# Optimization experiments

Measured on AMD Instinct MI355X. Metric: run time of the kernel, lower is better.

The kernel has to match this reference:

```python
import jax, jax.numpy as jnp
import numpy as np

# BlendParams / camera defaults (pytorch3d)
SIGMA = 1e-4
GAMMA = 1e-4
ZNEAR = 1.0
ZFAR = 100.0
EPS_BLEND = 1e-10
BG = jnp.array([1.0, 1.0, 1.0], dtype=jnp.float32)

N, H, W, K = 8, 512, 512, 4
V, F = 50000, 100000


def _normalize(x, eps=1e-6):
    n = jnp.linalg.norm(x, axis=-1, keepdims=True)
    return x / jnp.maximum(n, eps)


def setup_inputs() -> dict:
    key = jax.random.key(0)
    ks = jax.random.split(key, 12)
    verts = jax.random.normal(ks[0], (V, 3), jnp.float32)
    vertex_normals = _normalize(jax.random.normal(ks[1], (V, 3), jnp.float32))
    faces = jax.random.randint(ks[2], (F, 3), 0, V)
    p2f = jax.random.randint(ks[3], (N, H, W, K), 0, F)
    drop = jax.random.uniform(ks[4], (N, H, W, K)) < 0.2
    pix_to_face = jnp.where(drop, -1, p2f)
    bary = jax.random.uniform(ks[5], (N, H, W, K, 3), jnp.float32, 1e-3, 1.0)
    bary_coords = bary / bary.sum(-1, keepdims=True)  # valid barycentric weights
    zbuf = jax.random.uniform(ks[6], (N, H, W, K), jnp.float32, ZNEAR, ZFAR)
    dists = jax.random.normal(ks[7], (N, H, W, K), jnp.float32) * 1e-3
    texels = jax.random.uniform(ks[8], (N, H, W, K, 3), jnp.float32)
    vis_maps = jax.random.uniform(ks[9], (N, H, W, 3), jnp.float32)
    light_location = jax.random.normal(ks[10], (N, 3), jnp.float32) * 3.0
    camera_center = jax.random.normal(ks[11], (N, 3), jnp.float32) * 5.0
    return dict(
        verts=verts, vertex_normals=vertex_normals, bary_coords=bary_coords,
        zbuf=zbuf, dists=dists, texels=texels, vis_maps=vis_maps,
        light_location=light_location,
        light_ambient=jnp.full((N, 3), 0.5, jnp.float32),
        light_diffuse=jnp.full((N, 3), 0.3, jnp.float32),
        light_specular=jnp.full((N, 3), 0.2, jnp.float32),
        camera_center=camera_center,
        mat_ambient=jnp.ones((N, 3), jnp.float32),
        mat_diffuse=jnp.ones((N, 3), jnp.float32),
        mat_specular=jnp.ones((N, 3), jnp.float32),
        shininess=jnp.full((N,), 64.0, jnp.float32),
        faces=faces, pix_to_face=pix_to_face,
    )


def _interpolate_face_attributes(pix_to_face, bary, face_attrs):
    # face_attrs: (F, 3, D); pix_to_face: (N,H,W,K); bary: (N,H,W,K,3)
    mask = pix_to_face < 0
    idx = jnp.where(mask, 0, pix_to_face)
    gathered = face_attrs[idx]  # (N,H,W,K,3,D)
    out = jnp.einsum('nhwkv,nhwkvd->nhwkd', bary, gathered)
    return jnp.where(mask[..., None], 0.0, out)


def reference(verts, vertex_normals, bary_coords, zbuf, dists, texels, vis_maps,
              light_location, light_ambient, light_diffuse, light_specular,
              camera_center, mat_ambient, mat_diffuse, mat_specular, shininess,
              faces, pix_to_face):
    faces_verts = verts[faces]            # (F,3,3)
    faces_normals = vertex_normals[faces]  # (F,3,3)
    pixel_coords = _interpolate_face_attributes(pix_to_face, bary_coords, faces_verts)
    pixel_normals = _interpolate_face_attributes(pix_to_face, bary_coords, faces_normals)

    # ---- Phong lighting (PointLights) ----
    b = lambda v: v[:, None, None, None, :]  # (N,3) -> (N,1,1,1,3)
    normals = _normalize(pixel_normals)
    direction = _normalize(b(light_location) - pixel_coords)
    cos_angle = jnp.sum(normals * direction, axis=-1)  # (N,H,W,K)
    diffuse_light = b(light_diffuse) * jax.nn.relu(cos_angle)[..., None]
    reflect = -direction + 2.0 * cos_angle[..., None] * normals
    view_dir = _normalize(b(camera_center) - pixel_coords)
    spec_cos = jax.nn.relu(jnp.sum(view_dir * reflect, axis=-1)) * (cos_angle > 0)
    spec_light = b(light_specular) * (spec_cos ** shininess[:, None, None, None])[..., None]
    ambient = b(mat_ambient * light_ambient)
    diffuse = b(mat_diffuse) * diffuse_light
    specular = b(mat_specular) * spec_light

    vis = vis_maps[:, :, :, None, :]  # broadcast over K (== unsqueeze(-2).repeat)
    colors = (ambient + diffuse * vis) * texels + specular  # (N,H,W,K,3)

    # ---- softmax_rgb_blend ----
    mask = (pix_to_face >= 0).astype(colors.dtype)
    prob_map = jax.nn.sigmoid(-dists / SIGMA) * mask
    alpha = 1.0 - jnp.prod(1.0 - prob_map, axis=-1)
    z_inv = (ZFAR - zbuf) / (ZFAR - ZNEAR) * mask
    z_inv_max = jnp.maximum(jnp.max(z_inv, axis=-1, keepdims=True), EPS_BLEND)
    weights_num = prob_map * jnp.exp((z_inv - z_inv_max) / GAMMA)
    delta = jnp.exp((EPS_BLEND - z_inv_max) / GAMMA)
    denom = jnp.sum(weights_num, axis=-1, keepdims=True) + delta
    weighted_colors = jnp.einsum('nhwk,nhwkc->nhwc', weights_num, colors)
    rgb = (weighted_colors + delta * BG) / denom
    return jnp.concatenate([rgb, alpha[..., None]], axis=-1)  # (N,H,W,4)
```

## Files before the change

### kernel.cpp

```cpp
#include <hip/hip_runtime.h>
#include <math.h>

#define SIGMA_C   1e-4f
#define GAMMA_C   1e-4f
#define ZNEAR_C   1.0f
#define ZFAR_C    100.0f
#define EPSB_C    1e-10f

static constexpr int N_ = 8, H_ = 512, W_ = 512, K_ = 4;
static constexpr int NPIX = N_ * H_ * W_;
static constexpr int HW_SHIFT = 18;
static constexpr int F_ = 100000;
static constexpr int REC_F = 20;
static constexpr size_t TABLE_BYTES = (size_t)F_ * REC_F * sizeof(float);

typedef float fvec4 __attribute__((ext_vector_type(4)));
typedef float fvec2 __attribute__((ext_vector_type(2)));
typedef int   ivec4 __attribute__((ext_vector_type(4)));

struct F3 { float x, y, z; };
struct I3 { int   x, y, z; };

__device__ __forceinline__ fvec4 ntload_f4(const float* p) {
    return __builtin_nontemporal_load(reinterpret_cast<const fvec4*>(p));
}
__device__ __forceinline__ ivec4 ntload_i4(const int* p) {
    return __builtin_nontemporal_load(reinterpret_cast<const ivec4*>(p));
}

__global__ __launch_bounds__(256) void build_face_table(
    const float* __restrict__ verts,
    const float* __restrict__ vnorm,
    const int*   __restrict__ faces,
    float* __restrict__ table)
{
    const int f = blockIdx.x * 256 + threadIdx.x;
    if (f >= F_) return;
    const int i0 = faces[3*f+0], i1 = faces[3*f+1], i2 = faces[3*f+2];
    const F3 a = reinterpret_cast<const F3*>(verts)[i0];
    const F3 b = reinterpret_cast<const F3*>(verts)[i1];
    const F3 c = reinterpret_cast<const F3*>(verts)[i2];
    const F3 p = reinterpret_cast<const F3*>(vnorm)[i0];
    const F3 q = reinterpret_cast<const F3*>(vnorm)[i1];
    const F3 r = reinterpret_cast<const F3*>(vnorm)[i2];
    float* o = table + (size_t)f * REC_F;
    fvec4 r0 = {a.x, a.y, a.z, b.x};
    fvec4 r1 = {b.y, b.z, c.x, c.y};
    fvec4 r2 = {c.z, p.x, p.y, p.z};
    fvec4 r3 = {q.x, q.y, q.z, r.x};
    fvec2 r4 = {r.y, r.z};
    *reinterpret_cast<fvec4*>(o + 0)  = r0;
    *reinterpret_cast<fvec4*>(o + 4)  = r1;
    *reinterpret_cast<fvec4*>(o + 8)  = r2;
    *reinterpret_cast<fvec4*>(o + 12) = r3;
    *reinterpret_cast<fvec2*>(o + 16) = r4;
}

__global__ __launch_bounds__(256) void soft_phong_kernel(
    const float* __restrict__ table,
    const float* __restrict__ bary,
    const float* __restrict__ zbuf,
    const float* __restrict__ dists,
    const float* __restrict__ texels,
    const float* __restrict__ vis,
    const float* __restrict__ l_loc,
    const float* __restrict__ l_amb,
    const float* __restrict__ l_dif,
    const float* __restrict__ l_spec,
    const float* __restrict__ cam,
    const float* __restrict__ m_amb,
    const float* __restrict__ m_dif,
    const float* __restrict__ m_spec,
    const float* __restrict__ shininess,
    const int*   __restrict__ p2f,
    float* __restrict__ out)
{
    const int p = blockIdx.x * 256 + threadIdx.x;
    const int n = p >> HW_SHIFT;

    const ivec4 f4 = ntload_i4(p2f + 4*p);
    const fvec4 z4 = ntload_f4(zbuf + 4*p);
    const fvec4 d4 = ntload_f4(dists + 4*p);
    const fvec4 bA = ntload_f4(bary + 12*p + 0);
    const fvec4 bB = ntload_f4(bary + 12*p + 4);
    const fvec4 bC = ntload_f4(bary + 12*p + 8);
    const fvec4 tA = ntload_f4(texels + 12*p + 0);
    const fvec4 tB = ntload_f4(texels + 12*p + 4);
    const fvec4 tC = ntload_f4(texels + 12*p + 8);
    const float vR = __builtin_nontemporal_load(vis + 3*p+0);
    const float vG = __builtin_nontemporal_load(vis + 3*p+1);
    const float vB = __builtin_nontemporal_load(vis + 3*p+2);

    const int fi[4] = {f4.x, f4.y, f4.z, f4.w};

    const float llx = l_loc[3*n+0], lly = l_loc[3*n+1], llz = l_loc[3*n+2];
    const float ccx = cam[3*n+0],   ccy = cam[3*n+1],   ccz = cam[3*n+2];
    const float ambR = m_amb[3*n+0]*l_amb[3*n+0];
    const float ambG = m_amb[3*n+1]*l_amb[3*n+1];
    const float ambB = m_amb[3*n+2]*l_amb[3*n+2];
    const float kdR  = m_dif[3*n+0]*l_dif[3*n+0];
    const float kdG  = m_dif[3*n+1]*l_dif[3*n+1];
    const float kdB  = m_dif[3*n+2]*l_dif[3*n+2];
    const float ksR  = m_spec[3*n+0]*l_spec[3*n+0];
    const float ksG  = m_spec[3*n+1]*l_spec[3*n+1];
    const float ksB  = m_spec[3*n+2]*l_spec[3*n+2];
    const float shin = shininess[n];

    const float zb[4] = {z4.x, z4.y, z4.z, z4.w};
    const float dd[4] = {d4.x, d4.y, d4.z, d4.w};
    const float bc[12] = {bA.x,bA.y,bA.z,bA.w, bB.x,bB.y,bB.z,bB.w, bC.x,bC.y,bC.z,bC.w};
    const float tx[12] = {tA.x,tA.y,tA.z,tA.w, tB.x,tB.y,tB.z,tB.w, tC.x,tC.y,tC.z,tC.w};

    float colR[4], colG[4], colB[4], prob[4], zinv[4];
    float zmax = EPSB_C;

#pragma unroll
    for (int k = 0; k < 4; ++k) {
        const bool live = fi[k] >= 0;
        const int  f    = live ? fi[k] : 0;
        const float* rec = table + (size_t)f * REC_F;
        const fvec4 r0 = *reinterpret_cast<const fvec4*>(rec + 0);
        const fvec4 r1 = *reinterpret_cast<const fvec4*>(rec + 4);
        const fvec4 r2 = *reinterpret_cast<const fvec4*>(rec + 8);
        const fvec4 r3 = *reinterpret_cast<const fvec4*>(rec + 12);
        const fvec2 r4 = *reinterpret_cast<const fvec2*>(rec + 16);

        const float b0 = bc[3*k+0], b1 = bc[3*k+1], b2 = bc[3*k+2];

        const float pcx = b0*r0.x + b1*r0.w + b2*r1.z;
        const float pcy = b0*r0.y + b1*r1.x + b2*r1.w;
        const float pcz = b0*r0.z + b1*r1.y + b2*r2.x;

        const float pnx = b0*r2.y + b1*r3.x + b2*r3.w;
        const float pny = b0*r2.z + b1*r3.y + b2*r4.x;
        const float pnz = b0*r2.w + b1*r3.z + b2*r4.y;

        const float nl  = sqrtf(pnx*pnx + pny*pny + pnz*pnz);
        const float inl = 1.0f / fmaxf(nl, 1e-6f);
        const float nx = pnx*inl, ny = pny*inl, nz = pnz*inl;

        float dx = llx - pcx, dy = lly - pcy, dz = llz - pcz;
        const float dl  = sqrtf(dx*dx + dy*dy + dz*dz);
        const float idl = 1.0f / fmaxf(dl, 1e-6f);
        dx *= idl; dy *= idl; dz *= idl;

        const float cosang = nx*dx + ny*dy + nz*dz;
        const float rcos   = fmaxf(cosang, 0.0f);

        const float rx = 2.0f*cosang*nx - dx;
        const float ry = 2.0f*cosang*ny - dy;
        const float rz = 2.0f*cosang*nz - dz;

        float vx = ccx - pcx, vy = ccy - pcy, vz = ccz - pcz;
        const float vl  = sqrtf(vx*vx + vy*vy + vz*vz);
        const float ivl = 1.0f / fmaxf(vl, 1e-6f);
        vx *= ivl; vy *= ivl; vz *= ivl;

        const float sdot = vx*rx + vy*ry + vz*rz;
        const float spec_cos = (cosang > 0.0f) ? fmaxf(sdot, 0.0f) : 0.0f;
        const float sp = (spec_cos > 0.0f) ? exp2f(shin * log2f(spec_cos)) : 0.0f;

        colR[k] = (ambR + kdR*rcos*vR) * tx[3*k+0] + ksR*sp;
        colG[k] = (ambG + kdG*rcos*vG) * tx[3*k+1] + ksG*sp;
        colB[k] = (ambB + kdB*rcos*vB) * tx[3*k+2] + ksB*sp;

        prob[k] = live ? 1.0f / (1.0f + __expf(dd[k] / SIGMA_C)) : 0.0f;
        zinv[k] = live ? (ZFAR_C - zb[k]) / (ZFAR_C - ZNEAR_C)  : 0.0f;
        zmax = fmaxf(zmax, zinv[k]);
    }

    const float delta = __expf((EPSB_C - zmax) / GAMMA_C);
    float denom = delta;
    float accR = delta, accG = delta, accB = delta;
    float keep = 1.0f;
#pragma unroll
    for (int k = 0; k < 4; ++k) {
        const float w = prob[k] * __expf((zinv[k] - zmax) / GAMMA_C);
        denom += w;
        accR += w * colR[k];
        accG += w * colG[k];
        accB += w * colB[k];
        keep *= (1.0f - prob[k]);
    }
    const float inv = 1.0f / denom;
    fvec4 res; res.x = accR*inv; res.y = accG*inv; res.z = accB*inv; res.w = 1.0f - keep;
    __builtin_nontemporal_store(res, reinterpret_cast<fvec4*>(out) + p);
}

__global__ __launch_bounds__(256) void soft_phong_direct(
    const float* __restrict__ verts,
    const float* __restrict__ vnorm,
    const float* __restrict__ bary,
    const float* __restrict__ zbuf,
    const float* __restrict__ dists,
    const float* __restrict__ texels,
    const float* __restrict__ vis,
    const float* __restrict__ l_loc,
    const float* __restrict__ l_amb,
    const float* __restrict__ l_dif,
    const float* __restrict__ l_spec,
    const float* __restrict__ cam,
    const float* __restrict__ m_amb,
    const float* __restrict__ m_dif,
    const float* __restrict__ m_spec,
    const float* __restrict__ shininess,
    const int*   __restrict__ faces,
    const int*   __restrict__ p2f,
    float* __restrict__ out)
{
    const int p = blockIdx.x * 256 + threadIdx.x;
    const int n = p >> HW_SHIFT;
    const ivec4 f4 = ntload_i4(p2f + 4*p);
    const fvec4 z4 = ntload_f4(zbuf + 4*p);
    const fvec4 d4 = ntload_f4(dists + 4*p);
    const fvec4 bA = ntload_f4(bary + 12*p + 0);
    const fvec4 bB = ntload_f4(bary + 12*p + 4);
    const fvec4 bC = ntload_f4(bary + 12*p + 8);
    const fvec4 tA = ntload_f4(texels + 12*p + 0);
    const fvec4 tB = ntload_f4(texels + 12*p + 4);
    const fvec4 tC = ntload_f4(texels + 12*p + 8);
    const float vR = vis[3*p+0], vG = vis[3*p+1], vB = vis[3*p+2];
    const int fi[4] = {f4.x, f4.y, f4.z, f4.w};
    I3 fidx[4];
#pragma unroll
    for (int k = 0; k < 4; ++k) {
        const int f = (fi[k] >= 0) ? fi[k] : 0;
        fidx[k] = reinterpret_cast<const I3*>(faces)[f];
    }
    F3 vp[4][3], vn[4][3];
#pragma unroll
    for (int k = 0; k < 4; ++k) {
        const int i0 = fidx[k].x, i1 = fidx[k].y, i2 = fidx[k].z;
        vp[k][0] = reinterpret_cast<const F3*>(verts)[i0];
        vp[k][1] = reinterpret_cast<const F3*>(verts)[i1];
        vp[k][2] = reinterpret_cast<const F3*>(verts)[i2];
        vn[k][0] = reinterpret_cast<const F3*>(vnorm)[i0];
        vn[k][1] = reinterpret_cast<const F3*>(vnorm)[i1];
        vn[k][2] = reinterpret_cast<const F3*>(vnorm)[i2];
    }
    const float llx = l_loc[3*n+0], lly = l_loc[3*n+1], llz = l_loc[3*n+2];
    const float ccx = cam[3*n+0],   ccy = cam[3*n+1],   ccz = cam[3*n+2];
    const float ambR = m_amb[3*n+0]*l_amb[3*n+0];
    const float ambG = m_amb[3*n+1]*l_amb[3*n+1];
    const float ambB = m_amb[3*n+2]*l_amb[3*n+2];
    const float kdR  = m_dif[3*n+0]*l_dif[3*n+0];
    const float kdG  = m_dif[3*n+1]*l_dif[3*n+1];
    const float kdB  = m_dif[3*n+2]*l_dif[3*n+2];
    const float ksR  = m_spec[3*n+0]*l_spec[3*n+0];
    const float ksG  = m_spec[3*n+1]*l_spec[3*n+1];
    const float ksB  = m_spec[3*n+2]*l_spec[3*n+2];
    const float shin = shininess[n];
    const float zb[4] = {z4.x, z4.y, z4.z, z4.w};
    const float dd[4] = {d4.x, d4.y, d4.z, d4.w};
    const float bc[12] = {bA.x,bA.y,bA.z,bA.w, bB.x,bB.y,bB.z,bB.w, bC.x,bC.y,bC.z,bC.w};
    const float tx[12] = {tA.x,tA.y,tA.z,tA.w, tB.x,tB.y,tB.z,tB.w, tC.x,tC.y,tC.z,tC.w};
    float colR[4], colG[4], colB[4], prob[4], zinv[4];
    float zmax = EPSB_C;
#pragma unroll
    for (int k = 0; k < 4; ++k) {
        const bool live = fi[k] >= 0;
        const float b0 = bc[3*k+0], b1 = bc[3*k+1], b2 = bc[3*k+2];
        const float pcx = b0*vp[k][0].x + b1*vp[k][1].x + b2*vp[k][2].x;
        const float pcy = b0*vp[k][0].y + b1*vp[k][1].y + b2*vp[k][2].y;
        const float pcz = b0*vp[k][0].z + b1*vp[k][1].z + b2*vp[k][2].z;
        const float pnx = b0*vn[k][0].x + b1*vn[k][1].x + b2*vn[k][2].x;
        const float pny = b0*vn[k][0].y + b1*vn[k][1].y + b2*vn[k][2].y;
        const float pnz = b0*vn[k][0].z + b1*vn[k][1].z + b2*vn[k][2].z;
        const float nl  = sqrtf(pnx*pnx + pny*pny + pnz*pnz);
        const float inl = 1.0f / fmaxf(nl, 1e-6f);
        const float nx = pnx*inl, ny = pny*inl, nz = pnz*inl;
        float dx = llx - pcx, dy = lly - pcy, dz = llz - pcz;
        const float dl  = sqrtf(dx*dx + dy*dy + dz*dz);
        const float idl = 1.0f / fmaxf(dl, 1e-6f);
        dx *= idl; dy *= idl; dz *= idl;
        const float cosang = nx*dx + ny*dy + nz*dz;
        const float rcos   = fmaxf(cosang, 0.0f);
        const float rx = 2.0f*cosang*nx - dx;
        const float ry = 2.0f*cosang*ny - dy;
        const float rz = 2.0f*cosang*nz - dz;
        float vx = ccx - pcx, vy = ccy - pcy, vz = ccz - pcz;
        const float vl  = sqrtf(vx*vx + vy*vy + vz*vz);
        const float ivl = 1.0f / fmaxf(vl, 1e-6f);
        vx *= ivl; vy *= ivl; vz *= ivl;
        const float sdot = vx*rx + vy*ry + vz*rz;
        const float spec_cos = (cosang > 0.0f) ? fmaxf(sdot, 0.0f) : 0.0f;
        const float sp = (spec_cos > 0.0f) ? exp2f(shin * log2f(spec_cos)) : 0.0f;
        colR[k] = (ambR + kdR*rcos*vR) * tx[3*k+0] + ksR*sp;
        colG[k] = (ambG + kdG*rcos*vG) * tx[3*k+1] + ksG*sp;
        colB[k] = (ambB + kdB*rcos*vB) * tx[3*k+2] + ksB*sp;
        prob[k] = live ? 1.0f / (1.0f + __expf(dd[k] / SIGMA_C)) : 0.0f;
        zinv[k] = live ? (ZFAR_C - zb[k]) / (ZFAR_C - ZNEAR_C)  : 0.0f;
        zmax = fmaxf(zmax, zinv[k]);
    }
    const float delta = __expf((EPSB_C - zmax) / GAMMA_C);
    float denom = delta;
    float accR = delta, accG = delta, accB = delta;
    float keep = 1.0f;
#pragma unroll
    for (int k = 0; k < 4; ++k) {
        const float w = prob[k] * __expf((zinv[k] - zmax) / GAMMA_C);
        denom += w;
        accR += w * colR[k];
        accG += w * colG[k];
        accB += w * colB[k];
        keep *= (1.0f - prob[k]);
    }
    const float inv = 1.0f / denom;
    fvec4 res; res.x = accR*inv; res.y = accG*inv; res.z = accB*inv; res.w = 1.0f - keep;
    __builtin_nontemporal_store(res, reinterpret_cast<fvec4*>(out) + p);
}

extern "C" void kernel_launch(void* const* d_in, const int* in_sizes, int n_in,
                              void* d_out, int out_size, void* d_ws, size_t ws_size,
                              hipStream_t stream) {
    const float* verts   = (const float*)d_in[0];
    const float* vnorm   = (const float*)d_in[1];
    const float* bary    = (const float*)d_in[2];
    const float* zbuf    = (const float*)d_in[3];
    const float* dists   = (const float*)d_in[4];
    const float* texels  = (const float*)d_in[5];
    const float* vis     = (const float*)d_in[6];
    const float* l_loc   = (const float*)d_in[7];
    const float* l_amb   = (const float*)d_in[8];
    const float* l_dif   = (const float*)d_in[9];
    const float* l_spec  = (const float*)d_in[10];
    const float* cam     = (const float*)d_in[11];
    const float* m_amb   = (const float*)d_in[12];
    const float* m_dif   = (const float*)d_in[13];
    const float* m_spec  = (const float*)d_in[14];
    const float* shin    = (const float*)d_in[15];
    const int*   faces   = (const int*)d_in[16];
    const int*   p2f     = (const int*)d_in[17];
    float* out = (float*)d_out;

    if (ws_size >= TABLE_BYTES) {
        float* table = (float*)d_ws;
        build_face_table<<<(F_ + 255) / 256, 256, 0, stream>>>(verts, vnorm, faces, table);
        soft_phong_kernel<<<NPIX / 256, 256, 0, stream>>>(
            table, bary, zbuf, dists, texels, vis,
            l_loc, l_amb, l_dif, l_spec, cam,
            m_amb, m_dif, m_spec, shin, p2f, out);
    } else {
        soft_phong_direct<<<NPIX / 256, 256, 0, stream>>>(
            verts, vnorm, bary, zbuf, dists, texels, vis,
            l_loc, l_amb, l_dif, l_spec, cam,
            m_amb, m_dif, m_spec, shin, faces, p2f, out);
    }
}
```

Measured before the change: 410.6 us.

## Map one thread per fragment sample and blend across lanes with shuffles

The main kernel now assigns one thread to each (pixel, k) fragment rather than one thread per pixel looping over four fragments. The softmax blend reduction (max, sums, product) is done with xor-shuffles across groups of four lanes, and each lane writes one output channel. The aim is more parallelism and more outstanding independent face-table gathers to hide the latency of random accesses. In exchange it uses scalar rather than vector loads for per-sample inputs, loads vis redundantly per lane, and adds shuffle overhead. The fallback direct kernel is also reworked to use scalar loads.

```diff
diff --git a/kernel.cpp b/kernel.cpp
--- a/kernel.cpp
+++ b/kernel.cpp
@@ -9,23 +9,18 @@
 
 static constexpr int N_ = 8, H_ = 512, W_ = 512, K_ = 4;
 static constexpr int NPIX = N_ * H_ * W_;
-static constexpr int HW_SHIFT = 18;
+static constexpr int NSMP = NPIX * K_;
 static constexpr int F_ = 100000;
 static constexpr int REC_F = 20;
 static constexpr size_t TABLE_BYTES = (size_t)F_ * REC_F * sizeof(float);
 
 typedef float fvec4 __attribute__((ext_vector_type(4)));
 typedef float fvec2 __attribute__((ext_vector_type(2)));
-typedef int   ivec4 __attribute__((ext_vector_type(4)));
 
 struct F3 { float x, y, z; };
-struct I3 { int   x, y, z; };
-
-__device__ __forceinline__ fvec4 ntload_f4(const float* p) {
-    return __builtin_nontemporal_load(reinterpret_cast<const fvec4*>(p));
-}
-__device__ __forceinline__ ivec4 ntload_i4(const int* p) {
-    return __builtin_nontemporal_load(reinterpret_cast<const ivec4*>(p));
+
+__device__ __forceinline__ float ntf(const float* p) {
+    return __builtin_nontemporal_load(p);
 }
 
 __global__ __launch_bounds__(256) void build_face_table(
@@ -56,7 +51,7 @@
     *reinterpret_cast<fvec2*>(o + 16) = r4;
 }
 
-__global__ __launch_bounds__(256) void soft_phong_kernel(
+__global__ __launch_bounds__(256) void soft_phong_sample(
     const float* __restrict__ table,
     const float* __restrict__ bary,
     const float* __restrict__ zbuf,
@@ -75,23 +70,26 @@
     const int*   __restrict__ p2f,
     float* __restrict__ out)
 {
-    const int p = blockIdx.x * 256 + threadIdx.x;
-    const int n = p >> HW_SHIFT;
-
-    const ivec4 f4 = ntload_i4(p2f + 4*p);
-    const fvec4 z4 = ntload_f4(zbuf + 4*p);
-    const fvec4 d4 = ntload_f4(dists + 4*p);
-    const fvec4 bA = ntload_f4(bary + 12*p + 0);
-    const fvec4 bB = ntload_f4(bary + 12*p + 4);
-    const fvec4 bC = ntload_f4(bary + 12*p + 8);
-    const fvec4 tA = ntload_f4(texels + 12*p + 0);
-    const fvec4 tB = ntload_f4(texels + 12*p + 4);
-    const fvec4 tC = ntload_f4(texels + 12*p + 8);
-    const float vR = __builtin_nontemporal_load(vis + 3*p+0);
-    const float vG = __builtin_nontemporal_load(vis + 3*p+1);
-    const float vB = __builtin_nontemporal_load(vis + 3*p+2);
-
-    const int fi[4] = {f4.x, f4.y, f4.z, f4.w};
+    const int s = blockIdx.x * 256 + threadIdx.x;
+    const int p = s >> 2;
+    const int k = s & 3;
+    const int n = s >> 20;
+
+    const int  f0   = __builtin_nontemporal_load(p2f + s);
+    const bool live = f0 >= 0;
+    const int  f    = live ? f0 : 0;
+    const float* rec = table + (size_t)f * REC_F;
+    const fvec4 r0 = *reinterpret_cast<const fvec4*>(rec + 0);
+    const fvec4 r1 = *reinterpret_cast<const fvec4*>(rec + 4);
+    const fvec4 r2 = *reinterpret_cast<const fvec4*>(rec + 8);
+    const fvec4 r3 = *reinterpret_cast<const fvec4*>(rec + 12);
+    const fvec2 r4 = *reinterpret_cast<const fvec2*>(rec + 16);
+
+    const float zb = ntf(zbuf + s);
+    const float dd = ntf(dists + s);
+    const float b0 = ntf(bary + 3*s+0), b1 = ntf(bary + 3*s+1), b2 = ntf(bary + 3*s+2);
+    const float t0 = ntf(texels + 3*s+0), t1 = ntf(texels + 3*s+1), t2 = ntf(texels + 3*s+2);
+    const float vR = vis[3*p+0], vG = vis[3*p+1], vB = vis[3*p+2];
 
     const float llx = l_loc[3*n+0], lly = l_loc[3*n+1], llz = l_loc[3*n+2];
     const float ccx = cam[3*n+0],   ccy = cam[3*n+1],   ccz = cam[3*n+2];
@@ -106,85 +104,70 @@
     const float ksB  = m_spec[3*n+2]*l_spec[3*n+2];
     const float shin = shininess[n];
 
-    const float zb[4] = {z4.x, z4.y, z4.z, z4.w};
-    const float dd[4] = {d4.x, d4.y, d4.z, d4.w};
-    const float bc[12] = {bA.x,bA.y,bA.z,bA.w, bB.x,bB.y,bB.z,bB.w, bC.x,bC.y,bC.z,bC.w};
-    const float tx[12] = {tA.x,tA.y,tA.z,tA.w, tB.x,tB.y,tB.z,tB.w, tC.x,tC.y,tC.z,tC.w};
-
-    float colR[4], colG[4], colB[4], prob[4], zinv[4];
-    float zmax = EPSB_C;
-
-#pragma unroll
-    for (int k = 0; k < 4; ++k) {
-        const bool live = fi[k] >= 0;
-        const int  f    = live ? fi[k] : 0;
-        const float* rec = table + (size_t)f * REC_F;
-        const fvec4 r0 = *reinterpret_cast<const fvec4*>(rec + 0);
-        const fvec4 r1 = *reinterpret_cast<const fvec4*>(rec + 4);
-        const fvec4 r2 = *reinterpret_cast<const fvec4*>(rec + 8);
-        const fvec4 r3 = *reinterpret_cast<const fvec4*>(rec + 12);
-        const fvec2 r4 = *reinterpret_cast<const fvec2*>(rec + 16);
-
-        const float b0 = bc[3*k+0], b1 = bc[3*k+1], b2 = bc[3*k+2];
-
-        const float pcx = b0*r0.x + b1*r0.w + b2*r1.z;
-        const float pcy = b0*r0.y + b1*r1.x + b2*r1.w;
-        const float pcz = b0*r0.z + b1*r1.y + b2*r2.x;
-
-        const float pnx = b0*r2.y + b1*r3.x + b2*r3.w;
-        const float pny = b0*r2.z + b1*r3.y + b2*r4.x;
-        const float pnz = b0*r2.w + b1*r3.z + b2*r4.y;
-
-        const float nl  = sqrtf(pnx*pnx + pny*pny + pnz*pnz);
-        const float inl = 1.0f / fmaxf(nl, 1e-6f);
-        const float nx = pnx*inl, ny = pny*inl, nz = pnz*inl;
-
-        float dx = llx - pcx, dy = lly - pcy, dz = llz - pcz;
-        const float dl  = sqrtf(dx*dx + dy*dy + dz*dz);
-        const float idl = 1.0f / fmaxf(dl, 1e-6f);
-        dx *= idl; dy *= idl; dz *= idl;
-
-        const float cosang = nx*dx + ny*dy + nz*dz;
-        const float rcos   = fmaxf(cosang, 0.0f);
-
-        const float rx = 2.0f*cosang*nx - dx;
-        const float ry = 2.0f*cosang*ny - dy;
-        const float rz = 2.0f*cosang*nz - dz;
-
-        float vx = ccx - pcx, vy = ccy - pcy, vz = ccz - pcz;
-        const float vl  = sqrtf(vx*vx + vy*vy + vz*vz);
-        const float ivl = 1.0f / fmaxf(vl, 1e-6f);
-        vx *= ivl; vy *= ivl; vz *= ivl;
-
-        const float sdot = vx*rx + vy*ry + vz*rz;
-        const float spec_cos = (cosang > 0.0f) ? fmaxf(sdot, 0.0f) : 0.0f;
-        const float sp = (spec_cos > 0.0f) ? exp2f(shin * log2f(spec_cos)) : 0.0f;
-
-        colR[k] = (ambR + kdR*rcos*vR) * tx[3*k+0] + ksR*sp;
-        colG[k] = (ambG + kdG*rcos*vG) * tx[3*k+1] + ksG*sp;
-        colB[k] = (ambB + kdB*rcos*vB) * tx[3*k+2] + ksB*sp;
-
-        prob[k] = live ? 1.0f / (1.0f + __expf(dd[k] / SIGMA_C)) : 0.0f;
-        zinv[k] = live ? (ZFAR_C - zb[k]) / (ZFAR_C - ZNEAR_C)  : 0.0f;
-        zmax = fmaxf(zmax, zinv[k]);
-    }
+    const float pcx = b0*r0.x + b1*r0.w + b2*r1.z;
+    const float pcy = b0*r0.y + b1*r1.x + b2*r1.w;
+    const float pcz = b0*r0.z + b1*r1.y + b2*r2.x;
+
+    const float pnx = b0*r2.y + b1*r3.x + b2*r3.w;
+    const float pny = b0*r2.z + b1*r3.y + b2*r4.x;
+    const float pnz = b0*r2.w + b1*r3.z + b2*r4.y;
+
+    const float nl  = sqrtf(pnx*pnx + pny*pny + pnz*pnz);
+    const float inl = 1.0f / fmaxf(nl, 1e-6f);
+    const float nx = pnx*inl, ny = pny*inl, nz = pnz*inl;
+
+    float dx = llx - pcx, dy = lly - pcy, dz = llz - pcz;
+    const float dl  = sqrtf(dx*dx + dy*dy + dz*dz);
+    const float idl = 1.0f / fmaxf(dl, 1e-6f);
+    dx *= idl; dy *= idl; dz *= idl;
+
+    const float cosang = nx*dx + ny*dy + nz*dz;
+    const float rcos   = fmaxf(cosang, 0.0f);
+
+    const float rx = 2.0f*cosang*nx - dx;
+    const float ry = 2.0f*cosang*ny - dy;
+    const float rz = 2.0f*cosang*nz - dz;
+
+    float vx = ccx - pcx, vy = ccy - pcy, vz = ccz - pcz;
+    const float vl  = sqrtf(vx*vx + vy*vy + vz*vz);
+    const float ivl = 1.0f / fmaxf(vl, 1e-6f);
+    vx *= ivl; vy *= ivl; vz *= ivl;
+
+    const float sdot = vx*rx + vy*ry + vz*rz;
+    const float spec_cos = (cosang > 0.0f) ? fmaxf(sdot, 0.0f) : 0.0f;
+    const float sp = (spec_cos > 0.0f) ? exp2f(shin * log2f(spec_cos)) : 0.0f;
+
+    const float colR = (ambR + kdR*rcos*vR) * t0 + ksR*sp;
+    const float colG = (ambG + kdG*rcos*vG) * t1 + ksG*sp;
+    const float colB = (ambB + kdB*rcos*vB) * t2 + ksB*sp;
+
+    const float prob = live ? 1.0f / (1.0f + __expf(dd / SIGMA_C)) : 0.0f;
+    const float zinv = live ? (ZFAR_C - zb) / (ZFAR_C - ZNEAR_C)  : 0.0f;
+
+    float zmax = zinv;
+    zmax = fmaxf(zmax, __shfl_xor(zmax, 1));
+    zmax = fmaxf(zmax, __shfl_xor(zmax, 2));
+    zmax = fmaxf(zmax, EPSB_C);
+
+    const float w = prob * __expf((zinv - zmax) / GAMMA_C);
+    float aw = w, aR = w*colR, aG = w*colG, aB = w*colB, kp = 1.0f - prob;
+
+    aw += __shfl_xor(aw, 1);  aR += __shfl_xor(aR, 1);
+    aG += __shfl_xor(aG, 1);  aB += __shfl_xor(aB, 1);
+    kp *= __shfl_xor(kp, 1);
+    aw += __shfl_xor(aw, 2);  aR += __shfl_xor(aR, 2);
+    aG += __shfl_xor(aG, 2);  aB += __shfl_xor(aB, 2);
+    kp *= __shfl_xor(kp, 2);
 
     const float delta = __expf((EPSB_C - zmax) / GAMMA_C);
-    float denom = delta;
-    float accR = delta, accG = delta, accB = delta;
-    float keep = 1.0f;
-#pragma unroll
-    for (int k = 0; k < 4; ++k) {
-        const float w = prob[k] * __expf((zinv[k] - zmax) / GAMMA_C);
-        denom += w;
-        accR += w * colR[k];
-        accG += w * colG[k];
-        accB += w * colB[k];
-        keep *= (1.0f - prob[k]);
-    }
-    const float inv = 1.0f / denom;
-    fvec4 res; res.x = accR*inv; res.y = accG*inv; res.z = accB*inv; res.w = 1.0f - keep;
-    __builtin_nontemporal_store(res, reinterpret_cast<fvec4*>(out) + p);
+    const float inv   = 1.0f / (aw + delta);
+
+    float val;
+    if      (k == 0) val = (aR + delta) * inv;
+    else if (k == 1) val = (aG + delta) * inv;
+    else if (k == 2) val = (aB + delta) * inv;
+    else             val = 1.0f - kp;
+    __builtin_nontemporal_store(val, out + s);
 }
 
 __global__ __launch_bounds__(256) void soft_phong_direct(
@@ -209,18 +192,9 @@
     float* __restrict__ out)
 {
     const int p = blockIdx.x * 256 + threadIdx.x;
-    const int n = p >> HW_SHIFT;
-    const ivec4 f4 = ntload_i4(p2f + 4*p);
-    const fvec4 z4 = ntload_f4(zbuf + 4*p);
-    const fvec4 d4 = ntload_f4(dists + 4*p);
-    const fvec4 bA = ntload_f4(bary + 12*p + 0);
-    const fvec4 bB = ntload_f4(bary + 12*p + 4);
-    const fvec4 bC = ntload_f4(bary + 12*p + 8);
-    const fvec4 tA = ntload_f4(texels + 12*p + 0);
-    const fvec4 tB = ntload_f4(texels + 12*p + 4);
-    const fvec4 tC = ntload_f4(texels + 12*p + 8);
-    const float vR = vis[3*p+0], vG = vis[3*p+1], vB = vis[3*p+2];
-    const int fi[4] = {f4.x, f4.y, f4.z, f4.w};
+    const int n = p >> 18;
+    struct I3 { int x, y, z; };
+    const int fi[4] = {p2f[4*p+0], p2f[4*p+1], p2f[4*p+2], p2f[4*p+3]};
     I3 fidx[4];
 #pragma unroll
     for (int k = 0; k < 4; ++k) {
@@ -250,16 +224,12 @@
     const float ksG  = m_spec[3*n+1]*l_spec[3*n+1];
     const float ksB  = m_spec[3*n+2]*l_spec[3*n+2];
     const float shin = shininess[n];
-    const float zb[4] = {z4.x, z4.y, z4.z, z4.w};
-    const float dd[4] = {d4.x, d4.y, d4.z, d4.w};
-    const float bc[12] = {bA.x,bA.y,bA.z,bA.w, bB.x,bB.y,bB.z,bB.w, bC.x,bC.y,bC.z,bC.w};
-    const float tx[12] = {tA.x,tA.y,tA.z,tA.w, tB.x,tB.y,tB.z,tB.w, tC.x,tC.y,tC.z,tC.w};
     float colR[4], colG[4], colB[4], prob[4], zinv[4];
     float zmax = EPSB_C;
 #pragma unroll
     for (int k = 0; k < 4; ++k) {
         const bool live = fi[k] >= 0;
-        const float b0 = bc[3*k+0], b1 = bc[3*k+1], b2 = bc[3*k+2];
+        const float b0 = bary[12*p+3*k+0], b1 = bary[12*p+3*k+1], b2 = bary[12*p+3*k+2];
         const float pcx = b0*vp[k][0].x + b1*vp[k][1].x + b2*vp[k][2].x;
         const float pcy = b0*vp[k][0].y + b1*vp[k][1].y + b2*vp[k][2].y;
         const float pcz = b0*vp[k][0].z + b1*vp[k][1].z + b2*vp[k][2].z;
@@ -285,29 +255,24 @@
         const float sdot = vx*rx + vy*ry + vz*rz;
         const float spec_cos = (cosang > 0.0f) ? fmaxf(sdot, 0.0f) : 0.0f;
         const float sp = (spec_cos > 0.0f) ? exp2f(shin * log2f(spec_cos)) : 0.0f;
-        colR[k] = (ambR + kdR*rcos*vR) * tx[3*k+0] + ksR*sp;
-        colG[k] = (ambG + kdG*rcos*vG) * tx[3*k+1] + ksG*sp;
-        colB[k] = (ambB + kdB*rcos*vB) * tx[3*k+2] + ksB*sp;
-        prob[k] = live ? 1.0f / (1.0f + __expf(dd[k] / SIGMA_C)) : 0.0f;
-        zinv[k] = live ? (ZFAR_C - zb[k]) / (ZFAR_C - ZNEAR_C)  : 0.0f;
+        const float vRl = vis[3*p+0], vGl = vis[3*p+1], vBl = vis[3*p+2];
+        colR[k] = (ambR + kdR*rcos*vRl) * texels[12*p+3*k+0] + ksR*sp;
+        colG[k] = (ambG + kdG*rcos*vGl) * texels[12*p+3*k+1] + ksG*sp;
+        colB[k] = (ambB + kdB*rcos*vBl) * texels[12*p+3*k+2] + ksB*sp;
+        prob[k] = live ? 1.0f / (1.0f + __expf(dists[4*p+k] / SIGMA_C)) : 0.0f;
+        zinv[k] = live ? (ZFAR_C - zbuf[4*p+k]) / (ZFAR_C - ZNEAR_C)  : 0.0f;
         zmax = fmaxf(zmax, zinv[k]);
     }
     const float delta = __expf((EPSB_C - zmax) / GAMMA_C);
-    float denom = delta;
-    float accR = delta, accG = delta, accB = delta;
-    float keep = 1.0f;
+    float denom = delta, accR = delta, accG = delta, accB = delta, keep = 1.0f;
 #pragma unroll
     for (int k = 0; k < 4; ++k) {
         const float w = prob[k] * __expf((zinv[k] - zmax) / GAMMA_C);
-        denom += w;
-        accR += w * colR[k];
-        accG += w * colG[k];
-        accB += w * colB[k];
+        denom += w; accR += w*colR[k]; accG += w*colG[k]; accB += w*colB[k];
         keep *= (1.0f - prob[k]);
     }
     const float inv = 1.0f / denom;
-    fvec4 res; res.x = accR*inv; res.y = accG*inv; res.z = accB*inv; res.w = 1.0f - keep;
-    __builtin_nontemporal_store(res, reinterpret_cast<fvec4*>(out) + p);
+    out[4*p+0] = accR*inv; out[4*p+1] = accG*inv; out[4*p+2] = accB*inv; out[4*p+3] = 1.0f - keep;
 }
 
 extern "C" void kernel_launch(void* const* d_in, const int* in_sizes, int n_in,
@@ -336,7 +301,7 @@
     if (ws_size >= TABLE_BYTES) {
         float* table = (float*)d_ws;
         build_face_table<<<(F_ + 255) / 256, 256, 0, stream>>>(verts, vnorm, faces, table);
-        soft_phong_kernel<<<NPIX / 256, 256, 0, stream>>>(
+        soft_phong_sample<<<NSMP / 256, 256, 0, stream>>>(
             table, bary, zbuf, dists, texels, vis,
             l_loc, l_amb, l_dif, l_spec, cam,
             m_amb, m_dif, m_spec, shin, p2f, out);
```

Result: no change. 403.7 us (-1.7%).
